# Performance work log

Hardware: AMD Instinct MI355X
Metric: run time of the kernel (lower is better)

## Reference

```python
import jax, jax.numpy as jnp
import numpy as np

HEADS = 8
NBLK = 4  # N: 4x4 spatial blocks
DIM = 96
EPS_NORM = 1e-12  # torch F.normalize eps


def _blockify(t, head, n):
    # 'b (head c) (h1 hh) (w1 ww) -> b head c (h1 w1) (hh ww)'
    b, C, H, W = t.shape
    c, hh, ww = C // head, H // n, W // n
    t = t.reshape(b, head, c, n, hh, n, ww)
    return t.transpose(0, 1, 2, 3, 5, 4, 6).reshape(b, head, c, n * n, hh * ww)


def _unblockify(t, n, hh, ww):
    # inverse of _blockify
    b, head, c, _, _ = t.shape
    t = t.reshape(b, head, c, n, n, hh, ww).transpose(0, 1, 2, 3, 5, 4, 6)
    return t.reshape(b, head * c, n * hh, n * ww)


def _l2norm(t):
    return t / jnp.maximum(jnp.linalg.norm(t, axis=-1, keepdims=True), EPS_NORM)


def setup_inputs():
    key = jax.random.key(0)
    ks = jax.random.split(key, 5)
    b, dim, H, W = 4, DIM, 256, 256
    x = jax.random.normal(ks[0], (b, dim, H, W), jnp.float32)
    mask = jax.random.uniform(ks[1], (b, dim, H, W), jnp.float32)
    w_qkv = jax.random.normal(ks[2], (3 * dim, dim, 1, 1), jnp.float32) / np.sqrt(dim)
    w_dw = jax.random.normal(ks[3], (3 * dim, 1, 3, 3), jnp.float32) / 3.0
    w_proj = jax.random.normal(ks[4], (dim, dim, 1, 1), jnp.float32) / np.sqrt(dim)
    temp_x = jnp.ones((HEADS, 1, 1, 1), jnp.float32)
    temp_m = jnp.ones((HEADS, 1, 1, 1), jnp.float32)
    return {"x": x, "mask": mask, "w_qkv": w_qkv, "w_dw": w_dw,
            "w_proj": w_proj, "temp_x": temp_x, "temp_m": temp_m}


def reference(x, mask, w_qkv, w_dw, w_proj, temp_x, temp_m):
    # H, W chosen divisible by 4, so the reflect-pad in the original is a no-op.
    dn = ('NCHW', 'OIHW', 'NCHW')
    qkv = jax.lax.conv_general_dilated(x, w_qkv, (1, 1), 'VALID', dimension_numbers=dn)
    qkv = jax.lax.conv_general_dilated(qkv, w_dw, (1, 1), ((1, 1), (1, 1)),
                                       feature_group_count=qkv.shape[1],
                                       dimension_numbers=dn)
    q, k, v = jnp.split(qkv, 3, axis=1)
    q = _l2norm(_blockify(q, HEADS, NBLK))
    k = _l2norm(_blockify(k, HEADS, NBLK))
    v = _blockify(v, HEADS, NBLK)

    # channel-block attention: [b,head,c,16,16]; temp broadcasts over (b, c, 16, 16)
    attn_x = jax.nn.softmax(jnp.einsum('bhcns,bhcms->bhcnm', q, k) * temp_x, axis=-1)

    # mask-derived attention (MaskMap): q==k==blockified mask
    qm = _blockify(mask, HEADS, NBLK)
    attn_m = jnp.einsum('bhcns,bhcms->bhcnm', qm, qm) * temp_m
    attn_m = jax.nn.softmax(_l2norm(attn_m), axis=-1)

    attn = jax.nn.softmax(attn_x + attn_m, axis=-1)
    out = jnp.einsum('bhcnm,bhcms->bhcns', attn, v)

    hh, ww = x.shape[2] // NBLK, x.shape[3] // NBLK
    out = _unblockify(out, NBLK, hh, ww)
    out = jax.lax.conv_general_dilated(out, w_proj, (1, 1), 'VALID', dimension_numbers=dn)
    return out
```

## Files before the change

kernel.cpp:

```cpp
#include <hip/hip_runtime.h>
#include <math.h>

#define HPIX 256
#define WPIX 256
#define NPIX (HPIX * WPIX)
#define DIM 96
#define QKVC 288
#define NHEAD 8
#define CPH 12
#define EPSN 1e-12f
#define PSTRIDE 544

typedef __attribute__((ext_vector_type(8))) short bf16x8;
typedef __attribute__((ext_vector_type(4))) float f32x4;

__device__ __forceinline__ unsigned short f2bf(float f) {
  unsigned u = __float_as_uint(f);
  u += 0x7FFF + ((u >> 16) & 1);
  return (unsigned short)(u >> 16);
}
__device__ __forceinline__ float bf2f(unsigned short h) {
  return __uint_as_float((unsigned)h << 16);
}
__device__ __forceinline__ unsigned pkbf(float a, float b) {
  unsigned r;
  asm("v_cvt_pk_bf16_f32 %0, %1, %2" : "=v"(r) : "v"(a), "v"(b));
  return r;
}
__device__ __forceinline__ bf16x8 pack8(const float* f) {
  union { unsigned u[4]; bf16x8 v; } x;
  x.u[0] = pkbf(f[0], f[1]); x.u[1] = pkbf(f[2], f[3]);
  x.u[2] = pkbf(f[4], f[5]); x.u[3] = pkbf(f[6], f[7]);
  return x.v;
}

__global__ __launch_bounds__(256) void k_wprep(
    const float* __restrict__ wq, const float* __restrict__ wp,
    unsigned short* __restrict__ wqbf, unsigned short* __restrict__ wpbf) {
  int i = blockIdx.x * 256 + threadIdx.x;
  if (i < QKVC * DIM) wqbf[i] = f2bf(wq[i]);
  if (i < DIM * DIM)  wpbf[i] = f2bf(wp[i]);
}

template<int OC, int OCB, typename InT, typename OutT>
__global__ __launch_bounds__(256, (OCB > 96 ? 2 : 3)) void k_gemm1x1(
    const InT* __restrict__ xin, const unsigned short* __restrict__ wbf,
    OutT* __restrict__ out) {
  __shared__ __align__(16) unsigned short xT[128 * 128];
  __shared__ __align__(16) unsigned short wlds[OCB * 104];
  int t = threadIdx.x;
  int p0 = blockIdx.x * 128;
  int oc0 = blockIdx.y * OCB;
  const InT* xb = xin + (size_t)blockIdx.z * DIM * NPIX;

  for (int i = t; i < OCB * 12; i += 256) {
    int row = i / 12, seg = i % 12;
    bf16x8 w8 = *(const bf16x8*)(wbf + (size_t)(oc0 + row) * DIM + seg * 8);
    *(bf16x8*)&wlds[row * 104 + seg * 8] = w8;
  }
  if (t < 192) {
    int kg = t >> 4;
    int f4c = t & 15;
    #pragma unroll
    for (int rep = 0; rep < 2; ++rep) {
      int f4 = f4c + rep * 16;
      float vals[8][4];
      #pragma unroll
      for (int i = 0; i < 8; ++i) {
        if constexpr (sizeof(InT) == 2) {
          ushort4 v = *(const ushort4*)(xb + (size_t)(kg * 8 + i) * NPIX + p0 + f4 * 4);
          ((ushort*)vals[i])[0] = v.x; ((ushort*)vals[i])[1] = v.y;
          ((ushort*)vals[i])[2] = v.z; ((ushort*)vals[i])[3] = v.w;
        } else {
          float4 v = *(const float4*)(xb + (size_t)(kg * 8 + i) * NPIX + p0 + f4 * 4);
          vals[i][0] = v.x; vals[i][1] = v.y; vals[i][2] = v.z; vals[i][3] = v.w;
        }
      }
      #pragma unroll
      for (int c = 0; c < 4; ++c) {
        int px = f4 * 4 + c;
        int u = kg ^ ((px & 7) ^ ((px >> 3) & 7));
        bf16x8 hv;
        if constexpr (sizeof(InT) == 2) {
          #pragma unroll
          for (int i = 0; i < 8; ++i) hv[i] = (short)((ushort*)vals[i])[c];
        } else {
          float col[8];
          #pragma unroll
          for (int i = 0; i < 8; ++i) col[i] = vals[i][c];
          hv = pack8(col);
        }
        *(bf16x8*)&xT[px * 128 + u * 8] = hv;
      }
    }
  }
  __syncthreads();

  int lane = t & 63, wv = t >> 6;
  int r16 = lane & 15, kg8 = lane >> 4;

  bf16x8 bfr[3][2];
  #pragma unroll
  for (int nj = 0; nj < 2; ++nj) {
    int px = wv * 32 + nj * 16 + r16;
    int swz = (px & 7) ^ ((px >> 3) & 7);
    #pragma unroll
    for (int ks = 0; ks < 3; ++ks) {
      int u = (ks * 4 + kg8) ^ swz;
      bfr[ks][nj] = *(const bf16x8*)&xT[px * 128 + u * 8];
    }
  }

  f32x4 acc[OCB / 16][2];
  #pragma unroll
  for (int mi = 0; mi < OCB / 16; ++mi)
    #pragma unroll
    for (int nj = 0; nj < 2; ++nj) acc[mi][nj] = (f32x4){0.f, 0.f, 0.f, 0.f};

  #pragma unroll
  for (int mi = 0; mi < OCB / 16; ++mi) {
    #pragma unroll
    for (int ks = 0; ks < 3; ++ks) {
      bf16x8 a = *(const bf16x8*)&wlds[(mi * 16 + r16) * 104 + ks * 32 + kg8 * 8];
      #pragma unroll
      for (int nj = 0; nj < 2; ++nj)
        acc[mi][nj] = __builtin_amdgcn_mfma_f32_16x16x32_bf16(a, bfr[ks][nj], acc[mi][nj], 0, 0, 0);
    }
  }

  OutT* op = out + (size_t)blockIdx.z * OC * NPIX + p0;
  __syncthreads();
  if constexpr (sizeof(OutT) == 2) {
    unsigned short* tl = xT;
    #pragma unroll
    for (int mi = 0; mi < OCB / 16; ++mi)
      #pragma unroll
      for (int nj = 0; nj < 2; ++nj)
        #pragma unroll
        for (int j = 0; j < 4; ++j)
          tl[(mi * 16 + kg8 * 4 + j) * 136 + wv * 32 + nj * 16 + r16] = f2bf(acc[mi][nj][j]);
    __syncthreads();
    #pragma unroll
    for (int r = 0; r < OCB / 16; ++r) {
      int idx = t + 256 * r;
      int oc = idx >> 4, seg = idx & 15;
      bf16x8 v8 = *(const bf16x8*)&tl[oc * 136 + seg * 8];
      *(bf16x8*)(op + (size_t)(oc0 + oc) * NPIX + seg * 8) = v8;
    }
  } else {
    float* tl = (float*)xT;
    #pragma unroll
    for (int half = 0; half < 2; ++half) {
      if (half) __syncthreads();
      #pragma unroll
      for (int mi = half * (OCB / 32); mi < (half + 1) * (OCB / 32); ++mi)
        #pragma unroll
        for (int nj = 0; nj < 2; ++nj)
          #pragma unroll
          for (int j = 0; j < 4; ++j)
            tl[(mi * 16 + kg8 * 4 + j - half * (OCB / 2)) * 136 + wv * 32 + nj * 16 + r16]
                = acc[mi][nj][j];
      __syncthreads();
      #pragma unroll
      for (int r = 0; r < OCB / 16; ++r) {
        int idx = t + 256 * r;
        int oc = idx >> 5, seg = idx & 31;
        float4 v4 = *(const float4*)&tl[oc * 136 + seg * 4];
        *(float4*)(op + (size_t)(oc0 + half * (OCB / 2) + oc) * NPIX + seg * 4) = v4;
      }
    }
  }
}

__global__ __launch_bounds__(256) void k_dw3x3_bf(
    const unsigned short* __restrict__ in, const float* __restrict__ w,
    unsigned short* __restrict__ qkout, unsigned short* __restrict__ vout) {
  int t = threadIdx.x;
  int xg = t & 31, yp = t >> 5;
  int ybase = blockIdx.x * 16;
  int y0 = ybase + yp * 2;
  int x0 = xg * 8;
  int ch = blockIdx.y, b = blockIdx.z;
  const unsigned short* plane = in + ((size_t)b * QKVC + ch) * NPIX;
  const float* wc = w + ch * 9;

  float accA[8], accB[8];
  #pragma unroll
  for (int j = 0; j < 8; ++j) { accA[j] = 0.f; accB[j] = 0.f; }

  #pragma unroll
  for (int r = 0; r < 4; ++r) {
    int yy = y0 - 1 + r;
    float f[8];
    if (yy >= 0 && yy < HPIX) {
      bf16x8 v8 = *(const bf16x8*)(plane + (size_t)yy * WPIX + x0);
      #pragma unroll
      for (int j = 0; j < 8; ++j) f[j] = bf2f((unsigned short)v8[j]);
    } else {
      #pragma unroll
      for (int j = 0; j < 8; ++j) f[j] = 0.f;
    }
    float l = __shfl_up(f[7], 1);
    float rr = __shfl_down(f[0], 1);
    if (x0 == 0) l = 0.f;
    if (x0 == 248) rr = 0.f;
    if (r < 3) {
      float w0 = wc[r * 3], w1 = wc[r * 3 + 1], w2 = wc[r * 3 + 2];
      accA[0] = fmaf(w0, l, fmaf(w1, f[0], fmaf(w2, f[1], accA[0])));
      #pragma unroll
      for (int j = 1; j < 7; ++j)
        accA[j] = fmaf(w0, f[j - 1], fmaf(w1, f[j], fmaf(w2, f[j + 1], accA[j])));
      accA[7] = fmaf(w0, f[6], fmaf(w1, f[7], fmaf(w2, rr, accA[7])));
    }
    if (r > 0) {
      float w0 = wc[(r - 1) * 3], w1 = wc[(r - 1) * 3 + 1], w2 = wc[(r - 1) * 3 + 2];
      accB[0] = fmaf(w0, l, fmaf(w1, f[0], fmaf(w2, f[1], accB[0])));
      #pragma unroll
      for (int j = 1; j < 7; ++j)
        accB[j] = fmaf(w0, f[j - 1], fmaf(w1, f[j], fmaf(w2, f[j + 1], accB[j])));
      accB[7] = fmaf(w0, f[6], fmaf(w1, f[7], fmaf(w2, rr, accB[7])));
    }
  }

  bf16x8 oA = pack8(accA), oB = pack8(accB);
  size_t pA = (size_t)y0 * WPIX + x0;
  unsigned short* outp;
  if (ch < 192) outp = qkout + ((size_t)b * 192 + ch) * NPIX;
  else          outp = vout + ((size_t)b * DIM + ch - 192) * NPIX;
  *(bf16x8*)(outp + pA) = oA;
  *(bf16x8*)(outp + pA + WPIX) = oB;
}

__global__ __launch_bounds__(64) void k_attn_part(
    const unsigned short* __restrict__ qkbuf, const float* __restrict__ mask,
    float* __restrict__ pbuf) {
  int g = blockIdx.x, cb = blockIdx.y, lb = blockIdx.z;
  int lane = threadIdx.x;
  int r16 = lane & 15, kg8 = lane >> 4;

  const unsigned short* qb = qkbuf + ((size_t)lb * 192 + g) * NPIX;
  const unsigned short* kb = qkbuf + ((size_t)lb * 192 + 96 + g) * NPIX;
  const float* mb = mask + ((size_t)lb * DIM + g) * NPIX;

  int rbase = ((r16 >> 2) << 6) * WPIX + ((r16 & 3) << 6);

  f32x4 aqk = {0.f, 0.f, 0.f, 0.f}, amm = {0.f, 0.f, 0.f, 0.f};
  float dq = 0.f, dk = 0.f;

  #pragma unroll
  for (int ks = 0; ks < 8; ++ks) {
    int s = cb * 256 + ks * 32 + kg8 * 8;
    int off = rbase + (s >> 6) * WPIX + (s & 63);
    bf16x8 qf = *(const bf16x8*)(qb + off);
    bf16x8 kf = *(const bf16x8*)(kb + off);
    float4 m0 = *(const float4*)(mb + off);
    float4 m1 = *(const float4*)(mb + off + 4);
    union { unsigned u[4]; bf16x8 v; } mm_;
    mm_.u[0] = pkbf(m0.x, m0.y); mm_.u[1] = pkbf(m0.z, m0.w);
    mm_.u[2] = pkbf(m1.x, m1.y); mm_.u[3] = pkbf(m1.z, m1.w);
    bf16x8 mf = mm_.v;
    aqk = __builtin_amdgcn_mfma_f32_16x16x32_bf16(qf, kf, aqk, 0, 0, 0);
    amm = __builtin_amdgcn_mfma_f32_16x16x32_bf16(mf, mf, amm, 0, 0, 0);
    #pragma unroll
    for (int i = 0; i < 8; ++i) {
      float qv = bf2f((unsigned short)qf[i]); dq = fmaf(qv, qv, dq);
      float kv = bf2f((unsigned short)kf[i]); dk = fmaf(kv, kv, dk);
    }
  }
  dq += __shfl_xor(dq, 16); dq += __shfl_xor(dq, 32);
  dk += __shfl_xor(dk, 16); dk += __shfl_xor(dk, 32);

  float* pb = pbuf + (((size_t)lb * DIM + g) * 16 + cb) * PSTRIDE;
  #pragma unroll
  for (int j = 0; j < 4; ++j) {
    int n = kg8 * 4 + j;
    pb[n * 16 + r16] = aqk[j];
    pb[256 + n * 16 + r16] = amm[j];
  }
  if (lane < 16) { pb[512 + r16] = dq; pb[528 + r16] = dk; }
}

__global__ __launch_bounds__(256) void k_attn_fin(
    const float* __restrict__ pbuf, const float* __restrict__ tx,
    const float* __restrict__ tm, float* __restrict__ attnbuf) {
  int g = blockIdx.x;
  int lb = blockIdx.y;
  int h = g / CPH;
  int t = threadIdx.x;
  int n = t >> 4, m = t & 15;

  const float* pb = pbuf + ((size_t)lb * DIM + g) * 16 * PSTRIDE;
  float gqk = 0.f, gmm = 0.f, dq = 0.f, dk = 0.f;
  #pragma unroll
  for (int c = 0; c < 16; ++c) {
    const float* p = pb + c * PSTRIDE;
    gqk += p[t];
    gmm += p[256 + t];
    dq  += p[512 + n];
    dk  += p[528 + m];
  }

  float qn = fmaxf(sqrtf(dq), EPSN);
  float km = fmaxf(sqrtf(dk), EPSN);

  float ax = gqk / (qn * km) * tx[h];
  float r0 = ax;
  #pragma unroll
  for (int off = 8; off; off >>= 1) r0 = fmaxf(r0, __shfl_xor(r0, off, 16));
  float e0 = expf(ax - r0), es0 = e0;
  #pragma unroll
  for (int off = 8; off; off >>= 1) es0 += __shfl_xor(es0, off, 16);
  float attx = e0 / es0;

  float am = gmm * tm[h];
  float s2 = am * am;
  #pragma unroll
  for (int off = 8; off; off >>= 1) s2 += __shfl_xor(s2, off, 16);
  am = am / fmaxf(sqrtf(s2), EPSN);
  float r1 = am;
  #pragma unroll
  for (int off = 8; off; off >>= 1) r1 = fmaxf(r1, __shfl_xor(r1, off, 16));
  float e1 = expf(am - r1), es1 = e1;
  #pragma unroll
  for (int off = 8; off; off >>= 1) es1 += __shfl_xor(es1, off, 16);
  float attm = e1 / es1;

  float aa = attx + attm;
  float r2 = aa;
  #pragma unroll
  for (int off = 8; off; off >>= 1) r2 = fmaxf(r2, __shfl_xor(r2, off, 16));
  float e2 = expf(aa - r2), es2 = e2;
  #pragma unroll
  for (int off = 8; off; off >>= 1) es2 += __shfl_xor(es2, off, 16);

  attnbuf[(((size_t)lb * DIM + g) << 8) + t] = e2 / es2;
}

__global__ __launch_bounds__(256) void k_pv(
    const unsigned short* __restrict__ vbuf, const float* __restrict__ attnbuf,
    unsigned short* __restrict__ tout) {
  int hh = blockIdx.x;
  int g = blockIdx.y;
  int lb = blockIdx.z;
  int t = threadIdx.x;
  int ww = t & 63, grp = t >> 6;

  __shared__ float vt[16][64];
  __shared__ float at[16][16];

  const unsigned short* vb = vbuf + ((size_t)lb * DIM + g) * NPIX;
  #pragma unroll
  for (int jj = 0; jj < 4; ++jj) {
    int mm = jj * 4 + grp;
    vt[mm][ww] = bf2f(vb[(size_t)(((mm >> 2) << 6) + hh) * WPIX + ((mm & 3) << 6) + ww]);
  }
  at[t >> 4][t & 15] = attnbuf[(((size_t)lb * DIM + g) << 8) + t];
  __syncthreads();

  unsigned short* ob = tout + ((size_t)lb * DIM + g) * NPIX;
  #pragma unroll
  for (int jj = 0; jj < 4; ++jj) {
    int nn = jj * 4 + grp;
    float acc = 0.f;
    #pragma unroll
    for (int mm = 0; mm < 16; ++mm)
      acc = fmaf(at[nn][mm], vt[mm][ww], acc);
    ob[(size_t)(((nn >> 2) << 6) + hh) * WPIX + ((nn & 3) << 6) + ww] = f2bf(acc);
  }
}

extern "C" void kernel_launch(void* const* d_in, const int* in_sizes, int n_in,
                              void* d_out, int out_size, void* d_ws, size_t ws_size,
                              hipStream_t stream) {
  const float* x      = (const float*)d_in[0];
  const float* mask   = (const float*)d_in[1];
  const float* w_qkv  = (const float*)d_in[2];
  const float* w_dw   = (const float*)d_in[3];
  const float* w_proj = (const float*)d_in[4];
  const float* tx     = (const float*)d_in[5];
  const float* tm     = (const float*)d_in[6];
  float* out = (float*)d_out;

  const size_t wB     = (size_t)(QKVC * DIM + DIM * DIM) * 2;
  const size_t qkv1B  = (size_t)QKVC * NPIX * 2;
  const size_t qkB    = (size_t)192 * NPIX * 2;
  const size_t vB     = (size_t)DIM * NPIX * 2;
  const size_t atB    = (size_t)DIM * 256 * 4;
  const size_t pbB    = (size_t)DIM * 16 * PSTRIDE * 4;
  const size_t perB   = qkv1B + qkB + vB + atB + pbB;

  int nb = (ws_size >= wB + 4 * perB) ? 4 : 1;
  int npass = 4 / nb;

  char* base = (char*)d_ws;
  unsigned short* wqbf = (unsigned short*)base;
  unsigned short* wpbf = wqbf + QKVC * DIM;
  char* p = base + wB;
  unsigned short* qkv1bf = (unsigned short*)p;  p += (size_t)nb * qkv1B;
  unsigned short* tbuf   = qkv1bf;
  unsigned short* qkbuf  = (unsigned short*)p;  p += (size_t)nb * qkB;
  unsigned short* vbuf   = (unsigned short*)p;  p += (size_t)nb * vB;
  float*          attn   = (float*)p;           p += (size_t)nb * atB;
  float*          pbuf   = (float*)p;

  dim3 blk(256);
  k_wprep<<<dim3((QKVC * DIM + 255) / 256), blk, 0, stream>>>(
      w_qkv, w_proj, wqbf, wpbf);

  for (int pass = 0; pass < npass; ++pass) {
    int b0 = pass * nb;
    k_gemm1x1<QKVC, 144, float, unsigned short><<<dim3(NPIX / 128, 2, nb), blk, 0, stream>>>(
        x + (size_t)b0 * DIM * NPIX, wqbf, qkv1bf);
    k_dw3x3_bf<<<dim3(NPIX / 4096, QKVC, nb), blk, 0, stream>>>(
        qkv1bf, w_dw, qkbuf, vbuf);
    k_attn_part<<<dim3(DIM, 16, nb), dim3(64), 0, stream>>>(
        qkbuf, mask + (size_t)b0 * DIM * NPIX, pbuf);
    k_attn_fin<<<dim3(DIM, nb), blk, 0, stream>>>(pbuf, tx, tm, attn);
    k_pv<<<dim3(64, DIM, nb), blk, 0, stream>>>(vbuf, attn, tbuf);
    k_gemm1x1<DIM, 96, unsigned short, float><<<dim3(NPIX / 128, 1, nb), blk, 0, stream>>>(
        tbuf, wpbf, out + (size_t)b0 * DIM * NPIX);
  }
}
```

Before: 242.7 us.

## Fuse depthwise 3x3 conv for q/k into attention partial kernel

The depthwise 3x3 conv for the q and k channels now runs inside k_attn_part, reading the pre-conv 1x1 output directly. The standalone dw kernel handles only the v channels, and the intermediate q/k buffer is dropped. This removes a full write and read of 192 bf16 channel planes per batch. In exchange, attn_part does extra loads of three rows plus halo per element and more ALU work, with some redundant reads of neighbour rows.

```diff
diff --git a/kernel.cpp b/kernel.cpp
--- a/kernel.cpp
+++ b/kernel.cpp
@@ -32,6 +32,20 @@
   x.u[0] = pkbf(f[0], f[1]); x.u[1] = pkbf(f[2], f[3]);
   x.u[2] = pkbf(f[4], f[5]); x.u[3] = pkbf(f[6], f[7]);
   return x.v;
+}
+__device__ __forceinline__ void dw_accum(const unsigned short* rowp, int x,
+                                         float w0, float w1, float w2, float* o) {
+  bf16x8 c8 = *(const bf16x8*)(rowp + x);
+  float f[8];
+  #pragma unroll
+  for (int j = 0; j < 8; ++j) f[j] = bf2f((unsigned short)c8[j]);
+  float l = (x > 0) ? bf2f(rowp[x - 1]) : 0.f;
+  float r = (x < 248) ? bf2f(rowp[x + 8]) : 0.f;
+  o[0] = fmaf(w0, l, fmaf(w1, f[0], fmaf(w2, f[1], o[0])));
+  #pragma unroll
+  for (int j = 1; j < 7; ++j)
+    o[j] = fmaf(w0, f[j - 1], fmaf(w1, f[j], fmaf(w2, f[j + 1], o[j])));
+  o[7] = fmaf(w0, f[6], fmaf(w1, f[7], fmaf(w2, r, o[7])));
 }
 
 __global__ __launch_bounds__(256) void k_wprep(
@@ -174,15 +188,14 @@
 
 __global__ __launch_bounds__(256) void k_dw3x3_bf(
     const unsigned short* __restrict__ in, const float* __restrict__ w,
-    unsigned short* __restrict__ qkout, unsigned short* __restrict__ vout) {
+    unsigned short* __restrict__ vout) {
   int t = threadIdx.x;
   int xg = t & 31, yp = t >> 5;
-  int ybase = blockIdx.x * 16;
-  int y0 = ybase + yp * 2;
+  int y0 = blockIdx.x * 16 + yp * 2;
   int x0 = xg * 8;
   int ch = blockIdx.y, b = blockIdx.z;
-  const unsigned short* plane = in + ((size_t)b * QKVC + ch) * NPIX;
-  const float* wc = w + ch * 9;
+  const unsigned short* plane = in + ((size_t)b * QKVC + 192 + ch) * NPIX;
+  const float* wc = w + (192 + ch) * 9;
 
   float accA[8], accB[8];
   #pragma unroll
@@ -191,58 +204,35 @@
   #pragma unroll
   for (int r = 0; r < 4; ++r) {
     int yy = y0 - 1 + r;
-    float f[8];
     if (yy >= 0 && yy < HPIX) {
-      bf16x8 v8 = *(const bf16x8*)(plane + (size_t)yy * WPIX + x0);
-      #pragma unroll
-      for (int j = 0; j < 8; ++j) f[j] = bf2f((unsigned short)v8[j]);
-    } else {
-      #pragma unroll
-      for (int j = 0; j < 8; ++j) f[j] = 0.f;
-    }
-    float l = __shfl_up(f[7], 1);
-    float rr = __shfl_down(f[0], 1);
-    if (x0 == 0) l = 0.f;
-    if (x0 == 248) rr = 0.f;
-    if (r < 3) {
-      float w0 = wc[r * 3], w1 = wc[r * 3 + 1], w2 = wc[r * 3 + 2];
-      accA[0] = fmaf(w0, l, fmaf(w1, f[0], fmaf(w2, f[1], accA[0])));
-      #pragma unroll
-      for (int j = 1; j < 7; ++j)
-        accA[j] = fmaf(w0, f[j - 1], fmaf(w1, f[j], fmaf(w2, f[j + 1], accA[j])));
-      accA[7] = fmaf(w0, f[6], fmaf(w1, f[7], fmaf(w2, rr, accA[7])));
-    }
-    if (r > 0) {
-      float w0 = wc[(r - 1) * 3], w1 = wc[(r - 1) * 3 + 1], w2 = wc[(r - 1) * 3 + 2];
-      accB[0] = fmaf(w0, l, fmaf(w1, f[0], fmaf(w2, f[1], accB[0])));
-      #pragma unroll
-      for (int j = 1; j < 7; ++j)
-        accB[j] = fmaf(w0, f[j - 1], fmaf(w1, f[j], fmaf(w2, f[j + 1], accB[j])));
-      accB[7] = fmaf(w0, f[6], fmaf(w1, f[7], fmaf(w2, rr, accB[7])));
+      const unsigned short* row = plane + (size_t)yy * WPIX;
+      if (r < 3) dw_accum(row, x0, wc[r * 3], wc[r * 3 + 1], wc[r * 3 + 2], accA);
+      if (r > 0) dw_accum(row, x0, wc[(r - 1) * 3], wc[(r - 1) * 3 + 1], wc[(r - 1) * 3 + 2], accB);
     }
   }
 
   bf16x8 oA = pack8(accA), oB = pack8(accB);
+  unsigned short* outp = vout + ((size_t)b * DIM + ch) * NPIX;
   size_t pA = (size_t)y0 * WPIX + x0;
-  unsigned short* outp;
-  if (ch < 192) outp = qkout + ((size_t)b * 192 + ch) * NPIX;
-  else          outp = vout + ((size_t)b * DIM + ch - 192) * NPIX;
   *(bf16x8*)(outp + pA) = oA;
   *(bf16x8*)(outp + pA + WPIX) = oB;
 }
 
 __global__ __launch_bounds__(64) void k_attn_part(
-    const unsigned short* __restrict__ qkbuf, const float* __restrict__ mask,
-    float* __restrict__ pbuf) {
+    const unsigned short* __restrict__ qkv1, const float* __restrict__ wdw,
+    const float* __restrict__ mask, float* __restrict__ pbuf) {
   int g = blockIdx.x, cb = blockIdx.y, lb = blockIdx.z;
   int lane = threadIdx.x;
   int r16 = lane & 15, kg8 = lane >> 4;
 
-  const unsigned short* qb = qkbuf + ((size_t)lb * 192 + g) * NPIX;
-  const unsigned short* kb = qkbuf + ((size_t)lb * 192 + 96 + g) * NPIX;
+  const unsigned short* qp = qkv1 + ((size_t)lb * QKVC + g) * NPIX;
+  const unsigned short* kp = qkv1 + ((size_t)lb * QKVC + 96 + g) * NPIX;
   const float* mb = mask + ((size_t)lb * DIM + g) * NPIX;
-
-  int rbase = ((r16 >> 2) << 6) * WPIX + ((r16 & 3) << 6);
+  const float* wq9 = wdw + g * 9;
+  const float* wk9 = wdw + (96 + g) * 9;
+
+  int ybase = (r16 >> 2) << 6;
+  int xbase = (r16 & 3) << 6;
 
   f32x4 aqk = {0.f, 0.f, 0.f, 0.f}, amm = {0.f, 0.f, 0.f, 0.f};
   float dq = 0.f, dk = 0.f;
@@ -250,15 +240,30 @@
   #pragma unroll
   for (int ks = 0; ks < 8; ++ks) {
     int s = cb * 256 + ks * 32 + kg8 * 8;
-    int off = rbase + (s >> 6) * WPIX + (s & 63);
-    bf16x8 qf = *(const bf16x8*)(qb + off);
-    bf16x8 kf = *(const bf16x8*)(kb + off);
+    int y = ybase + (s >> 6);
+    int x = xbase + (s & 63);
+    int off = y * WPIX + x;
+
+    float oq[8], ok[8];
+    #pragma unroll
+    for (int j = 0; j < 8; ++j) { oq[j] = 0.f; ok[j] = 0.f; }
+    #pragma unroll
+    for (int r = 0; r < 3; ++r) {
+      int yy = y - 1 + r;
+      if (yy < 0 || yy >= HPIX) continue;
+      dw_accum(qp + (size_t)yy * WPIX, x, wq9[r * 3], wq9[r * 3 + 1], wq9[r * 3 + 2], oq);
+      dw_accum(kp + (size_t)yy * WPIX, x, wk9[r * 3], wk9[r * 3 + 1], wk9[r * 3 + 2], ok);
+    }
+    bf16x8 qf = pack8(oq);
+    bf16x8 kf = pack8(ok);
+
     float4 m0 = *(const float4*)(mb + off);
     float4 m1 = *(const float4*)(mb + off + 4);
     union { unsigned u[4]; bf16x8 v; } mm_;
     mm_.u[0] = pkbf(m0.x, m0.y); mm_.u[1] = pkbf(m0.z, m0.w);
     mm_.u[2] = pkbf(m1.x, m1.y); mm_.u[3] = pkbf(m1.z, m1.w);
     bf16x8 mf = mm_.v;
+
     aqk = __builtin_amdgcn_mfma_f32_16x16x32_bf16(qf, kf, aqk, 0, 0, 0);
     amm = __builtin_amdgcn_mfma_f32_16x16x32_bf16(mf, mf, amm, 0, 0, 0);
     #pragma unroll
@@ -383,11 +388,10 @@
 
   const size_t wB     = (size_t)(QKVC * DIM + DIM * DIM) * 2;
   const size_t qkv1B  = (size_t)QKVC * NPIX * 2;
-  const size_t qkB    = (size_t)192 * NPIX * 2;
   const size_t vB     = (size_t)DIM * NPIX * 2;
   const size_t atB    = (size_t)DIM * 256 * 4;
   const size_t pbB    = (size_t)DIM * 16 * PSTRIDE * 4;
-  const size_t perB   = qkv1B + qkB + vB + atB + pbB;
+  const size_t perB   = qkv1B + vB + atB + pbB;
 
   int nb = (ws_size >= wB + 4 * perB) ? 4 : 1;
   int npass = 4 / nb;
@@ -398,7 +402,6 @@
   char* p = base + wB;
   unsigned short* qkv1bf = (unsigned short*)p;  p += (size_t)nb * qkv1B;
   unsigned short* tbuf   = qkv1bf;
-  unsigned short* qkbuf  = (unsigned short*)p;  p += (size_t)nb * qkB;
   unsigned short* vbuf   = (unsigned short*)p;  p += (size_t)nb * vB;
   float*          attn   = (float*)p;           p += (size_t)nb * atB;
   float*          pbuf   = (float*)p;
@@ -411,10 +414,10 @@
     int b0 = pass * nb;
     k_gemm1x1<QKVC, 144, float, unsigned short><<<dim3(NPIX / 128, 2, nb), blk, 0, stream>>>(
         x + (size_t)b0 * DIM * NPIX, wqbf, qkv1bf);
-    k_dw3x3_bf<<<dim3(NPIX / 4096, QKVC, nb), blk, 0, stream>>>(
-        qkv1bf, w_dw, qkbuf, vbuf);
+    k_dw3x3_bf<<<dim3(NPIX / 4096, DIM, nb), blk, 0, stream>>>(
+        qkv1bf, w_dw, vbuf);
     k_attn_part<<<dim3(DIM, 16, nb), dim3(64), 0, stream>>>(
-        qkbuf, mask + (size_t)b0 * DIM * NPIX, pbuf);
+        qkv1bf, w_dw, mask + (size_t)b0 * DIM * NPIX, pbuf);
     k_attn_fin<<<dim3(DIM, nb), blk, 0, stream>>>(pbuf, tx, tm, attn);
     k_pv<<<dim3(64, DIM, nb), blk, 0, stream>>>(vbuf, attn, tbuf);
     k_gemm1x1<DIM, 96, unsigned short, float><<<dim3(NPIX / 128, 1, nb), blk, 0, stream>>>(
```

Result: slower. 312.9 us (+28.9%).
